# Kernel optimization log

Hardware: AMD Instinct MI355X
Metric: run time of the kernel (lower is better)

Reference implementation:

```python
import jax, jax.numpy as jnp
import numpy as np

EPS = 1e-5

def _ln(v, gamma, beta):
    mu = jnp.mean(v, axis=-1, keepdims=True)
    var = jnp.mean(jnp.square(v - mu), axis=-1, keepdims=True)
    return (v - mu) * jax.lax.rsqrt(var + EPS) * gamma + beta

def setup_inputs() -> dict:
    B, T, D = 8, 2048, 2048
    NG = 3  # n_strands - 1
    key = jax.random.key(0)
    ks = jax.random.split(key, 8)
    s = lambda k, shp, fan: jax.random.normal(k, shp, jnp.float32) * (1.0 / np.sqrt(fan))
    return {
        "x": jax.random.normal(ks[0], (B, T, D), jnp.float32),
        "W1": s(ks[1], (D, 2 * D), 2 * D), "b1": jnp.zeros((D,), jnp.float32),
        "W2": s(ks[2], (2 * NG, D), D), "b2": jnp.zeros((2 * NG,), jnp.float32),
        "Wp": s(ks[3], (D, D), D), "bp": jnp.zeros((D,), jnp.float32),
        "gamma": jnp.ones((D,), jnp.float32), "beta": jnp.zeros((D,), jnp.float32),
    }

def reference(x, W1, b1, W2, b2, Wp, bp, gamma, beta):
    # Adjacent-pair crossing features: pair_t = [x_t, x_{t+1}], t = 0..T-2
    pair = jnp.concatenate([x[:, :-1], x[:, 1:]], axis=-1)          # (B,T-1,2D)
    h = jax.nn.gelu(jnp.einsum('btk,dk->btd', pair, W1) + b1, approximate=False)
    logits = jnp.einsum('btd,gd->btg', h, W2) + b2                   # (B,T-1,2*NG)
    scale = jnp.mean(jax.nn.softmax(logits, axis=-1), axis=-1, keepdims=True)  # (B,T-1,1)
    P = jnp.einsum('btd,ed->bte', x, Wp) + bp                        # mix_proj(x)
    m = P[:, 1:] * scale    # added to position t at step t
    mp = P[:, :-1] * scale  # added to position t+1 at step t
    # Loop semantics: pos t first updated as j at step t-1, then as i at step t.
    tmp = jnp.concatenate([x[:, :1], _ln(x[:, 1:] + mp, gamma, beta)], axis=1)
    out = jnp.concatenate([_ln(tmp[:, :-1] + m, gamma, beta), tmp[:, -1:]], axis=1)
    return out
```

## Files before the change

### kernel.cpp

```cpp
#include <hip/hip_runtime.h>
#include <hip/hip_bf16.h>
#include <stdint.h>


#define B_DIM 8
#define T_DIM 2048
#define D_DIM 2048
#define M_DIM (B_DIM * T_DIM)
#define N_DIM D_DIM
#define K_DIM D_DIM

typedef __attribute__((ext_vector_type(8))) short short8;
typedef __attribute__((ext_vector_type(4))) float f32x4;

__device__ inline unsigned short f2bf(float f) {
    unsigned u = __float_as_uint(f);
    u += 0x7fffu + ((u >> 16) & 1u);
    return (unsigned short)(u >> 16);
}
__device__ inline float bf2f(unsigned u16) {
    return __uint_as_float(u16 << 16);
}
__device__ inline void unpack8(uint4 u, float* f) {
    f[0] = bf2f(u.x & 0xffffu); f[1] = bf2f(u.x >> 16);
    f[2] = bf2f(u.y & 0xffffu); f[3] = bf2f(u.y >> 16);
    f[4] = bf2f(u.z & 0xffffu); f[5] = bf2f(u.z >> 16);
    f[6] = bf2f(u.w & 0xffffu); f[7] = bf2f(u.w >> 16);
}

__device__ inline void async_ld16(const void* g, void* l) {
    __builtin_amdgcn_global_load_lds(
        (__attribute__((address_space(1))) void*)(g),
        (__attribute__((address_space(3))) void*)(l),
        16, 0, 0);
}

__global__ void cast_f32_bf16(const float* __restrict__ x, unsigned short* __restrict__ Xb,
                              const float* __restrict__ Wp, unsigned short* __restrict__ Wb,
                              int nx4, int ntot4) {
    int i = blockIdx.x * blockDim.x + threadIdx.x;
    if (i >= ntot4) return;
    const float* src; unsigned short* dst; int j;
    if (i < nx4) { src = x; dst = Xb; j = i; }
    else         { src = Wp; dst = Wb; j = i - nx4; }
    float4 f = ((const float4*)src)[j];
    ushort4 o;
    o.x = f2bf(f.x); o.y = f2bf(f.y); o.z = f2bf(f.z); o.w = f2bf(f.w);
    ((ushort4*)dst)[j] = o;
}

__global__ void gemm_bt(const unsigned short* __restrict__ Xb,
                        const unsigned short* __restrict__ Wb,
                        const float* __restrict__ bp,
                        unsigned short* __restrict__ P)
{
    __shared__ unsigned short As[128 * 64];
    __shared__ unsigned short Bs[128 * 64];

    const int tid  = threadIdx.x;
    const int lane = tid & 63;
    const int wave = tid >> 6;
    const int m0 = blockIdx.y * 128;
    const int n0 = blockIdx.x * 128;

    const int rw = (wave >> 1) * 64;
    const int cw = (wave & 1) * 64;
    const int fr = lane & 15;
    const int lq = lane >> 4;

    int s_r[4], s_l[4], s_ci[4];
#pragma unroll
    for (int q = 0; q < 4; q++) {
        int ci = (wave * 4 + q) * 64 + lane;
        s_ci[q] = ci;
        s_r[q] = ci >> 3;
        s_l[q] = (ci & 7) ^ (s_r[q] & 7);
    }

    f32x4 acc[4][4];
#pragma unroll
    for (int i = 0; i < 4; i++)
#pragma unroll
        for (int j = 0; j < 4; j++) acc[i][j] = (f32x4){0.f, 0.f, 0.f, 0.f};

    for (int k0 = 0; k0 < K_DIM; k0 += 64) {
#pragma unroll
        for (int q = 0; q < 4; q++) {
            async_ld16(Xb + (size_t)(m0 + s_r[q]) * K_DIM + k0 + s_l[q] * 8,
                       As + s_ci[q] * 8);
            async_ld16(Wb + (size_t)(n0 + s_r[q]) * K_DIM + k0 + s_l[q] * 8,
                       Bs + s_ci[q] * 8);
        }
        __syncthreads();

#pragma unroll
        for (int kk = 0; kk < 2; kk++) {
            const int l = kk * 4 + lq;
            short8 a[4], b[4];
#pragma unroll
            for (int i = 0; i < 4; i++) {
                int row = rw + 16 * i + fr;
                a[i] = *(const short8*)(As + row * 64 + (l ^ (row & 7)) * 8);
            }
#pragma unroll
            for (int j = 0; j < 4; j++) {
                int row = cw + 16 * j + fr;
                b[j] = *(const short8*)(Bs + row * 64 + (l ^ (row & 7)) * 8);
            }
#pragma unroll
            for (int i = 0; i < 4; i++)
#pragma unroll
                for (int j = 0; j < 4; j++)
                    acc[i][j] = __builtin_amdgcn_mfma_f32_16x16x32_bf16(a[i], b[j], acc[i][j], 0, 0, 0);
        }
        __syncthreads();
    }

    const int crow = (lane >> 4) * 4;
    const int ccol = lane & 15;
#pragma unroll
    for (int j = 0; j < 4; j++) {
        int col = n0 + cw + 16 * j + ccol;
        float bpv = bp[col];
#pragma unroll
        for (int i = 0; i < 4; i++) {
            size_t base = (size_t)(m0 + rw + 16 * i + crow) * N_DIM + col;
#pragma unroll
            for (int r = 0; r < 4; r++)
                P[base + (size_t)r * N_DIM] = f2bf(acc[i][j][r] + bpv);
        }
    }
}

__device__ inline void ln_stage(float* v, const float* g, const float* be, float* sm, int tid) {
    float s = 0.f, q = 0.f;
#pragma unroll
    for (int i = 0; i < 8; i++) { s += v[i]; q += v[i] * v[i]; }
#pragma unroll
    for (int off = 32; off; off >>= 1) { s += __shfl_down(s, off); q += __shfl_down(q, off); }
    int w = tid >> 6;
    if ((tid & 63) == 0) { sm[w * 2] = s; sm[w * 2 + 1] = q; }
    __syncthreads();
    s = sm[0] + sm[2] + sm[4] + sm[6];
    q = sm[1] + sm[3] + sm[5] + sm[7];
    __syncthreads();
    const float invD = 1.0f / (float)D_DIM;
    float mu = s * invD;
    float var = q * invD - mu * mu;
    float rs = rsqrtf(var + 1e-5f);
#pragma unroll
    for (int i = 0; i < 8; i++) v[i] = (v[i] - mu) * rs * g[i] + be[i];
}

__global__ void ln_kernel(const unsigned short* __restrict__ Xb,
                          const unsigned short* __restrict__ P,
                          const float* __restrict__ gamma,
                          const float* __restrict__ beta,
                          float* __restrict__ out)
{
    const int r = blockIdx.x;
    const int t = r & (T_DIM - 1);
    const int tid = threadIdx.x;
    __shared__ float sm[8];

    float v[8], g[8], be[8];
    unpack8(((const uint4*)(Xb + (size_t)r * D_DIM))[tid], v);
    {
        float4 g0 = ((const float4*)gamma)[2 * tid], g1 = ((const float4*)gamma)[2 * tid + 1];
        g[0] = g0.x; g[1] = g0.y; g[2] = g0.z; g[3] = g0.w;
        g[4] = g1.x; g[5] = g1.y; g[6] = g1.z; g[7] = g1.w;
        float4 b0 = ((const float4*)beta)[2 * tid], b1 = ((const float4*)beta)[2 * tid + 1];
        be[0] = b0.x; be[1] = b0.y; be[2] = b0.z; be[3] = b0.w;
        be[4] = b1.x; be[5] = b1.y; be[6] = b1.z; be[7] = b1.w;
    }

    const float inv6 = 1.0f / 6.0f;

    if (t > 0) {
        float p[8];
        unpack8(((const uint4*)(P + (size_t)(r - 1) * D_DIM))[tid], p);
#pragma unroll
        for (int i = 0; i < 8; i++) v[i] += p[i] * inv6;
        ln_stage(v, g, be, sm, tid);
    }
    if (t < T_DIM - 1) {
        float p[8];
        unpack8(((const uint4*)(P + (size_t)(r + 1) * D_DIM))[tid], p);
#pragma unroll
        for (int i = 0; i < 8; i++) v[i] += p[i] * inv6;
        ln_stage(v, g, be, sm, tid);
    }

    float4* orow = (float4*)(out + (size_t)r * D_DIM);
    orow[2 * tid]     = (float4){v[0], v[1], v[2], v[3]};
    orow[2 * tid + 1] = (float4){v[4], v[5], v[6], v[7]};
}

extern "C" void kernel_launch(void* const* d_in, const int* in_sizes, int n_in,
                              void* d_out, int out_size, void* d_ws, size_t ws_size,
                              hipStream_t stream) {
    const float* x     = (const float*)d_in[0];
    const float* Wp    = (const float*)d_in[5];
    const float* bp    = (const float*)d_in[6];
    const float* gamma = (const float*)d_in[7];
    const float* beta  = (const float*)d_in[8];
    float* out = (float*)d_out;

    unsigned short* Xb = (unsigned short*)d_ws;
    unsigned short* Wb = Xb + (size_t)M_DIM * K_DIM;
    unsigned short* P  = Wb + (size_t)N_DIM * K_DIM;

    const int nx4   = (M_DIM * K_DIM) / 4;
    const int ntot4 = nx4 + (N_DIM * K_DIM) / 4;
    cast_f32_bf16<<<(ntot4 + 255) / 256, 256, 0, stream>>>(x, Xb, Wp, Wb, nx4, ntot4);

    dim3 ggrid(N_DIM / 128, M_DIM / 128);
    gemm_bt<<<ggrid, 256, 0, stream>>>(Xb, Wb, bp, P);
    ln_kernel<<<M_DIM, 256, 0, stream>>>(Xb, P, gamma, beta, out);
}
```

Before: 421.1 us.

## Process LayerNorm rows per wave with rolling P-row reuse and grid-stride cast

The LayerNorm kernel now assigns 8 consecutive rows to each wave and keeps the previous, current and next rows of P in registers, so each P row is loaded once instead of twice. Reductions use wave-wide xor shuffles with no shared memory or block barriers. The cast kernel becomes a grid-stride loop over a fixed 4096-block grid, and the GEMM epilogue is reordered so stores walk along rows. The cost is higher register pressure (32 floats each for values, gamma and beta per thread) and fewer, longer-running blocks in the LN kernel.

Measured after the change: 426.6 us. About the same (+1.3%).

```diff
diff --git a/kernel.cpp b/kernel.cpp
--- a/kernel.cpp
+++ b/kernel.cpp
@@ -1,5 +1,4 @@
 #include <hip/hip_runtime.h>
-#include <hip/hip_bf16.h>
 #include <stdint.h>
 
 
@@ -9,6 +8,7 @@
 #define M_DIM (B_DIM * T_DIM)
 #define N_DIM D_DIM
 #define K_DIM D_DIM
+#define LROWS 8
 
 typedef __attribute__((ext_vector_type(8))) short short8;
 typedef __attribute__((ext_vector_type(4))) float f32x4;
@@ -27,7 +27,6 @@
     f[4] = bf2f(u.z & 0xffffu); f[5] = bf2f(u.z >> 16);
     f[6] = bf2f(u.w & 0xffffu); f[7] = bf2f(u.w >> 16);
 }
-
 __device__ inline void async_ld16(const void* g, void* l) {
     __builtin_amdgcn_global_load_lds(
         (__attribute__((address_space(1))) void*)(g),
@@ -38,15 +37,16 @@
 __global__ void cast_f32_bf16(const float* __restrict__ x, unsigned short* __restrict__ Xb,
                               const float* __restrict__ Wp, unsigned short* __restrict__ Wb,
                               int nx4, int ntot4) {
-    int i = blockIdx.x * blockDim.x + threadIdx.x;
-    if (i >= ntot4) return;
-    const float* src; unsigned short* dst; int j;
-    if (i < nx4) { src = x; dst = Xb; j = i; }
-    else         { src = Wp; dst = Wb; j = i - nx4; }
-    float4 f = ((const float4*)src)[j];
-    ushort4 o;
-    o.x = f2bf(f.x); o.y = f2bf(f.y); o.z = f2bf(f.z); o.w = f2bf(f.w);
-    ((ushort4*)dst)[j] = o;
+    for (int i = blockIdx.x * blockDim.x + threadIdx.x; i < ntot4;
+         i += gridDim.x * blockDim.x) {
+        const float* src; unsigned short* dst; int j;
+        if (i < nx4) { src = x; dst = Xb; j = i; }
+        else         { src = Wp; dst = Wb; j = i - nx4; }
+        float4 f = ((const float4*)src)[j];
+        ushort4 o;
+        o.x = f2bf(f.x); o.y = f2bf(f.y); o.z = f2bf(f.z); o.w = f2bf(f.w);
+        ((ushort4*)dst)[j] = o;
+    }
 }
 
 __global__ void gemm_bt(const unsigned short* __restrict__ Xb,
@@ -118,82 +118,125 @@
 
     const int crow = (lane >> 4) * 4;
     const int ccol = lane & 15;
-#pragma unroll
-    for (int j = 0; j < 4; j++) {
-        int col = n0 + cw + 16 * j + ccol;
-        float bpv = bp[col];
-#pragma unroll
-        for (int i = 0; i < 4; i++) {
-            size_t base = (size_t)(m0 + rw + 16 * i + crow) * N_DIM + col;
-#pragma unroll
-            for (int r = 0; r < 4; r++)
-                P[base + (size_t)r * N_DIM] = f2bf(acc[i][j][r] + bpv);
-        }
-    }
-}
-
-__device__ inline void ln_stage(float* v, const float* g, const float* be, float* sm, int tid) {
+    float bpv[4];
+#pragma unroll
+    for (int j = 0; j < 4; j++) bpv[j] = bp[n0 + cw + 16 * j + ccol];
+#pragma unroll
+    for (int i = 0; i < 4; i++) {
+#pragma unroll
+        for (int r = 0; r < 4; r++) {
+            size_t base = (size_t)(m0 + rw + 16 * i + crow + r) * N_DIM
+                        + n0 + cw + ccol;
+#pragma unroll
+            for (int j = 0; j < 4; j++)
+                P[base + 16 * j] = f2bf(acc[i][j][r] + bpv[j]);
+        }
+    }
+}
+
+__device__ __attribute__((always_inline)) inline
+void ln_wave(float (&v)[32], const float (&g)[32], const float (&be)[32], int lane) {
     float s = 0.f, q = 0.f;
 #pragma unroll
-    for (int i = 0; i < 8; i++) { s += v[i]; q += v[i] * v[i]; }
-#pragma unroll
-    for (int off = 32; off; off >>= 1) { s += __shfl_down(s, off); q += __shfl_down(q, off); }
-    int w = tid >> 6;
-    if ((tid & 63) == 0) { sm[w * 2] = s; sm[w * 2 + 1] = q; }
-    __syncthreads();
-    s = sm[0] + sm[2] + sm[4] + sm[6];
-    q = sm[1] + sm[3] + sm[5] + sm[7];
-    __syncthreads();
+    for (int i = 0; i < 32; ++i) { s += v[i]; q += v[i] * v[i]; }
+#pragma unroll
+    for (int off = 32; off; off >>= 1) {
+        s += __shfl_xor(s, off);
+        q += __shfl_xor(q, off);
+    }
     const float invD = 1.0f / (float)D_DIM;
-    float mu = s * invD;
-    float var = q * invD - mu * mu;
-    float rs = rsqrtf(var + 1e-5f);
-#pragma unroll
-    for (int i = 0; i < 8; i++) v[i] = (v[i] - mu) * rs * g[i] + be[i];
-}
-
-__global__ void ln_kernel(const unsigned short* __restrict__ Xb,
-                          const unsigned short* __restrict__ P,
-                          const float* __restrict__ gamma,
-                          const float* __restrict__ beta,
-                          float* __restrict__ out)
+    const float mu = s * invD;
+    const float rs = rsqrtf(q * invD - mu * mu + 1e-5f);
+#pragma unroll
+    for (int i = 0; i < 32; ++i) v[i] = (v[i] - mu) * rs * g[i] + be[i];
+}
+
+__global__ __launch_bounds__(256, 2)
+void ln_kernel(const unsigned short* __restrict__ Xb,
+               const unsigned short* __restrict__ P,
+               const float* __restrict__ gamma,
+               const float* __restrict__ beta,
+               float* __restrict__ out)
 {
-    const int r = blockIdx.x;
-    const int t = r & (T_DIM - 1);
-    const int tid = threadIdx.x;
-    __shared__ float sm[8];
-
-    float v[8], g[8], be[8];
-    unpack8(((const uint4*)(Xb + (size_t)r * D_DIM))[tid], v);
+    const int lane = threadIdx.x & 63;
+    const int w = blockIdx.x * 4 + (threadIdx.x >> 6);
+    const int r0 = w * LROWS;
+    const int t0 = r0 & (T_DIM - 1);
+    const float inv6 = 1.0f / 6.0f;
+
+    float g[32], be[32];
     {
-        float4 g0 = ((const float4*)gamma)[2 * tid], g1 = ((const float4*)gamma)[2 * tid + 1];
-        g[0] = g0.x; g[1] = g0.y; g[2] = g0.z; g[3] = g0.w;
-        g[4] = g1.x; g[5] = g1.y; g[6] = g1.z; g[7] = g1.w;
-        float4 b0 = ((const float4*)beta)[2 * tid], b1 = ((const float4*)beta)[2 * tid + 1];
-        be[0] = b0.x; be[1] = b0.y; be[2] = b0.z; be[3] = b0.w;
-        be[4] = b1.x; be[5] = b1.y; be[6] = b1.z; be[7] = b1.w;
-    }
-
-    const float inv6 = 1.0f / 6.0f;
-
-    if (t > 0) {
-        float p[8];
-        unpack8(((const uint4*)(P + (size_t)(r - 1) * D_DIM))[tid], p);
-#pragma unroll
-        for (int i = 0; i < 8; i++) v[i] += p[i] * inv6;
-        ln_stage(v, g, be, sm, tid);
-    }
-    if (t < T_DIM - 1) {
-        float p[8];
-        unpack8(((const uint4*)(P + (size_t)(r + 1) * D_DIM))[tid], p);
-#pragma unroll
-        for (int i = 0; i < 8; i++) v[i] += p[i] * inv6;
-        ln_stage(v, g, be, sm, tid);
-    }
-
-    float4* orow = (float4*)(out + (size_t)r * D_DIM);
-    orow[2 * tid]     = (float4){v[0], v[1], v[2], v[3]};
-    orow[2 * tid + 1] = (float4){v[4], v[5], v[6], v[7]};
+        const float4* g4 = (const float4*)gamma;
+        const float4* b4 = (const float4*)beta;
+#pragma unroll
+        for (int c = 0; c < 4; ++c) {
+            const int e = (c * 64 + lane) * 2;
+            float4 g0 = g4[e], g1 = g4[e + 1];
+            float4 b0 = b4[e], b1 = b4[e + 1];
+            g[c*8+0]=g0.x; g[c*8+1]=g0.y; g[c*8+2]=g0.z; g[c*8+3]=g0.w;
+            g[c*8+4]=g1.x; g[c*8+5]=g1.y; g[c*8+6]=g1.z; g[c*8+7]=g1.w;
+            be[c*8+0]=b0.x; be[c*8+1]=b0.y; be[c*8+2]=b0.z; be[c*8+3]=b0.w;
+            be[c*8+4]=b1.x; be[c*8+5]=b1.y; be[c*8+6]=b1.z; be[c*8+7]=b1.w;
+        }
+    }
+
+    const uint4* Pq = (const uint4*)P;
+    uint4 pm[4], pc[4], pn[4];
+    {
+        const int rm = (t0 > 0) ? r0 - 1 : r0;
+#pragma unroll
+        for (int c = 0; c < 4; ++c) pm[c] = Pq[(size_t)rm * 256 + c * 64 + lane];
+#pragma unroll
+        for (int c = 0; c < 4; ++c) pc[c] = Pq[(size_t)r0 * 256 + c * 64 + lane];
+    }
+
+    for (int tt = 0; tt < LROWS; ++tt) {
+        const int r = r0 + tt;
+        const int t = t0 + tt;
+
+        const int rn = (t < T_DIM - 1) ? r + 1 : r;
+#pragma unroll
+        for (int c = 0; c < 4; ++c) pn[c] = Pq[(size_t)rn * 256 + c * 64 + lane];
+
+        float v[32];
+        const uint4* xq = (const uint4*)Xb + (size_t)r * 256;
+#pragma unroll
+        for (int c = 0; c < 4; ++c) {
+            float f[8]; unpack8(xq[c * 64 + lane], f);
+#pragma unroll
+            for (int jj = 0; jj < 8; ++jj) v[c * 8 + jj] = f[jj];
+        }
+
+        if (t > 0) {
+#pragma unroll
+            for (int c = 0; c < 4; ++c) {
+                float f[8]; unpack8(pm[c], f);
+#pragma unroll
+                for (int jj = 0; jj < 8; ++jj) v[c * 8 + jj] += f[jj] * inv6;
+            }
+            ln_wave(v, g, be, lane);
+        }
+        if (t < T_DIM - 1) {
+#pragma unroll
+            for (int c = 0; c < 4; ++c) {
+                float f[8]; unpack8(pn[c], f);
+#pragma unroll
+                for (int jj = 0; jj < 8; ++jj) v[c * 8 + jj] += f[jj] * inv6;
+            }
+            ln_wave(v, g, be, lane);
+        }
+
+        float4* orow = (float4*)(out + (size_t)r * D_DIM);
+#pragma unroll
+        for (int c = 0; c < 4; ++c) {
+            const int e = (c * 64 + lane) * 2;
+            orow[e]     = (float4){v[c*8+0], v[c*8+1], v[c*8+2], v[c*8+3]};
+            orow[e + 1] = (float4){v[c*8+4], v[c*8+5], v[c*8+6], v[c*8+7]};
+        }
+
+#pragma unroll
+        for (int c = 0; c < 4; ++c) { pm[c] = pc[c]; pc[c] = pn[c]; }
+    }
 }
 
 extern "C" void kernel_launch(void* const* d_in, const int* in_sizes, int n_in,
@@ -212,9 +255,10 @@
 
     const int nx4   = (M_DIM * K_DIM) / 4;
     const int ntot4 = nx4 + (N_DIM * K_DIM) / 4;
-    cast_f32_bf16<<<(ntot4 + 255) / 256, 256, 0, stream>>>(x, Xb, Wp, Wb, nx4, ntot4);
+    cast_f32_bf16<<<4096, 256, 0, stream>>>(x, Xb, Wp, Wb, nx4, ntot4);
 
     dim3 ggrid(N_DIM / 128, M_DIM / 128);
     gemm_bt<<<ggrid, 256, 0, stream>>>(Xb, Wb, bp, P);
-    ln_kernel<<<M_DIM, 256, 0, stream>>>(Xb, P, gamma, beta, out);
-}
+
+    ln_kernel<<<(M_DIM / LROWS) / 4, 256, 0, stream>>>(Xb, P, gamma, beta, out);
+}
```
